# Performance work log

Measured on AMD Instinct MI355X. Metric: run time of the kernel, lower is better.

Reference implementation:

```python
import jax, jax.numpy as jnp
import numpy as np

ALPHA = 0.2      # leaky_relu negative slope
EPS = 1e-5       # BatchNorm eps
NEG = -9e15      # masked attention fill (matches -9000000000000000.0)


def _xavier(key, shape):
    fan_in, fan_out = shape[-2], shape[-1]
    lim = jnp.sqrt(6.0 / (fan_in + fan_out))
    return jax.random.uniform(key, shape, minval=-lim, maxval=lim, dtype=jnp.float32)


def setup_inputs() -> dict:
    key = jax.random.key(0)
    ks = jax.random.split(key, 10)
    b, N, L = 8, 1024, 4
    C, G, O, F = 128, 128, 64, 64   # n_feats, global_feats, global_out_feats, n_filters
    V = jax.random.normal(ks[0], (b, N, C), dtype=jnp.float32)
    A = jax.random.normal(ks[1], (b, N, L, N), dtype=jnp.float32)
    global_state = jax.random.normal(ks[2], (b, G), dtype=jnp.float32)
    graph_size = jax.random.randint(ks[3], (b,), 0, N, dtype=jnp.int32)
    subgraph_size = jax.random.randint(ks[4], (b, 1), 0, N, dtype=jnp.int32)
    Wg = _xavier(ks[5], (G, O))                 # broadcast_global_state.weights[0]
    W = _xavier(ks[6], (L, C + O, F))           # GAT per-channel weight_list
    a1 = _xavier(ks[7], (L, F, 1))
    a2 = _xavier(ks[8], (L, F, 1))
    bias_gat = jnp.full((F,), 0.01, dtype=jnp.float32)
    gamma_n = jnp.ones((F,), jnp.float32); beta_n = jnp.zeros((F,), jnp.float32)
    gamma_g = jnp.ones((O,), jnp.float32); beta_g = jnp.zeros((O,), jnp.float32)
    return dict(V=V, A=A, global_state=global_state, graph_size=graph_size,
                subgraph_size=subgraph_size, Wg=Wg, W=W, a1=a1, a2=a2,
                bias_gat=bias_gat, gamma_n=gamma_n, beta_n=beta_n,
                gamma_g=gamma_g, beta_g=beta_g)


def reference(V, A, global_state, graph_size, subgraph_size,
              Wg, W, a1, a2, bias_gat, gamma_n, beta_n, gamma_g, beta_g):
    b, N, C = V.shape
    # --- GraphNodeCatGlobalFeatures (mols=1): project global state, broadcast to
    # the first graph_size[i] nodes of each graph, zeros for padding nodes.
    gs = global_state @ Wg                                   # [b, O]
    node_mask = (jnp.arange(N)[None, :] < graph_size[:, None]).astype(V.dtype)  # [b, N]
    Vg = jnp.concatenate([V, gs[:, None, :] * node_mask[:, :, None]], axis=-1)  # [b, N, C+O]
    # --- GraphAttentionLayer, all adj channels vectorized. dropout=0.
    h = jnp.einsum('bnc,lcf->lbnf', Vg, W)                   # [L, b, N, F]
    f1 = jnp.einsum('lbnf,lf->lbn', h, a1[:, :, 0])          # [L, b, N]
    f2 = jnp.einsum('lbnf,lf->lbn', h, a2[:, :, 0])
    e = jax.nn.leaky_relu(f1[:, :, :, None] + f2[:, :, None, :], ALPHA)  # [L, b, N, N]
    adj = jnp.transpose(A, (2, 0, 1, 3))                     # [L, b, N, N]
    att = jnp.where(adj > 0, e, jnp.asarray(NEG, e.dtype))
    att = jax.nn.softmax(att, axis=2)                        # torch softmax dim=1 (row index)
    out = jnp.einsum('lbnm,lbmf->bnf', att, h) + bias_gat    # sum over channels, [b, N, F]
    # --- bn_graph (BatchNorm1d over feature channel, training-mode batch stats) + relu
    mu = out.mean(axis=(0, 1))
    var = out.var(axis=(0, 1))
    out = jax.nn.relu((out - mu) / jnp.sqrt(var + EPS) * gamma_n + beta_n)
    # --- bn_global + relu on the projected global state
    gmu = gs.mean(axis=0)
    gvar = gs.var(axis=0)
    gs_out = jax.nn.relu((gs - gmu) / jnp.sqrt(gvar + EPS) * gamma_g + beta_g)
    return (out, gs_out)
```

## Files before the change

kernel.cpp:

```cpp
#include <hip/hip_runtime.h>
#include <hip/hip_fp16.h>

typedef unsigned long long u64;
typedef unsigned short ushort_t;
typedef __attribute__((ext_vector_type(8))) short short8v;
typedef __attribute__((ext_vector_type(16))) float f32x16;

#define DI __device__ __forceinline__

DI unsigned cvt_pk_bf16(float lo, float hi) {
    unsigned r;
    asm volatile("v_cvt_pk_bf16_f32 %0, %1, %2" : "=v"(r) : "v"(lo), "v"(hi));
    return r;
}

__global__ __launch_bounds__(256)
void k_h(const float* V, const int* gsize, const float* gstate, const float* Wg,
         const float* W, const float* a1, const float* a2,
         ushort_t* hT, float* f1, float* f2)
{
    int blk = blockIdx.x;
    int b = blk >> 5, nt = blk & 31, n0 = nt * 32;
    int t = threadIdx.x;
    __shared__ float gss[64];
    __shared__ float was[2][4][192];
    __shared__ float vg[32][194];
    if (t < 64) {
        float acc = 0.f;
        for (int c = 0; c < 128; ++c) acc += gstate[b*128 + c] * Wg[c*64 + t];
        gss[t] = acc;
    } else {
        int tt = t - 64;
        #pragma unroll
        for (int k = 0; k < 8; ++k) {
            int e = tt + k*192;
            int which = (e >= 768) ? 1 : 0;
            int idx = which ? e - 768 : e;
            int l = idx / 192, c = idx - l*192;
            const float* ap = (which ? a2 : a1) + l*64;
            const float* wp = W + (l*192 + c) * 64;
            float s = 0.f;
            for (int f = 0; f < 64; ++f) s += wp[f] * ap[f];
            was[which][l][c] = s;
        }
    }
    __syncthreads();
    {
        int r = t >> 3, c0 = (t & 7) * 16;
        const float* vp = V + ((size_t)(b*1024 + n0 + r) * 128 + c0);
        float4 v0 = *(const float4*)(vp + 0);
        float4 v1 = *(const float4*)(vp + 4);
        float4 v2 = *(const float4*)(vp + 8);
        float4 v3 = *(const float4*)(vp + 12);
        *(float4*)&vg[r][c0 + 0]  = v0;
        *(float4*)&vg[r][c0 + 4]  = v1;
        *(float4*)&vg[r][c0 + 8]  = v2;
        *(float4*)&vg[r][c0 + 12] = v3;
    }
    {
        int r = t >> 3, o0 = (t & 7) * 8;
        bool on = (n0 + r) < gsize[b];
        for (int j = 0; j < 8; ++j) vg[r][128 + o0 + j] = on ? gss[o0 + j] : 0.f;
    }
    __syncthreads();
    int ty = t >> 5, tx = t & 31;
    int r0 = ty * 4;
    int j0 = tx * 8;
    int lw = j0 >> 6, f0 = j0 & 63;
    float acc[4][8];
    for (int i = 0; i < 4; ++i) for (int j = 0; j < 8; ++j) acc[i][j] = 0.f;
    const float* wp = W + (size_t)(lw*192) * 64 + f0;
    for (int c = 0; c < 192; ++c) {
        float4 wl = *(const float4*)(wp + c*64);
        float4 wh = *(const float4*)(wp + c*64 + 4);
        float wf[8] = {wl.x, wl.y, wl.z, wl.w, wh.x, wh.y, wh.z, wh.w};
        float a0 = vg[r0+0][c], a1v = vg[r0+1][c], a2v = vg[r0+2][c], a3v = vg[r0+3][c];
        for (int j = 0; j < 8; ++j) {
            acc[0][j] += a0  * wf[j];
            acc[1][j] += a1v * wf[j];
            acc[2][j] += a2v * wf[j];
            acc[3][j] += a3v * wf[j];
        }
    }
    int lb = lw*8 + b;
    #pragma unroll
    for (int j = 0; j < 8; ++j) {
        uint2 st;
        st.x = cvt_pk_bf16(acc[0][j], acc[1][j]);
        st.y = cvt_pk_bf16(acc[2][j], acc[3][j]);
        *(uint2*)(hT + ((size_t)(lb*64 + f0 + j)) * 1024 + n0 + r0) = st;
    }
    {
        int r = t & 31, l = (t >> 5) & 3, which = t >> 7;
        const float* wl = &was[which][l][0];
        float s = 0.f;
        for (int c = 0; c < 192; ++c) s += vg[r][c] * wl[c];
        float* dst = which ? f2 : f1;
        dst[(l*8 + b) * 1024 + n0 + r] = s;
    }
}

__global__ __launch_bounds__(256, 2)
void k_maskcolsum(const float* A, const float* f1, const float* f2,
                  u64* maskp, float* psum)
{
    int blk = blockIdx.x;
    int nc = blk & 15, l = (blk >> 4) & 3, b = blk >> 6;
    int t = threadIdx.x;
    int wv = t >> 6, lane = t & 63;
    int lb = l*8 + b;
    int n0 = nc*64 + wv*16;
    ushort_t* mp16 = (ushort_t*)maskp;

    float K[16], F2r[16];
    {
        const float* f2p = f2 + lb*1024 + lane*16;
        #pragma unroll
        for (int q = 0; q < 4; ++q) {
            float4 v = *(const float4*)(f2p + q*4);
            float x4[4] = {v.x, v.y, v.z, v.w};
            #pragma unroll
            for (int i = 0; i < 4; ++i) {
                F2r[q*4 + i] = x4[i];
                K[q*4 + i]   = fmaxf(x4[i], 0.2f*x4[i]) + 12.f;
            }
        }
    }
    float f1r[16];
    {
        const float* f1p = f1 + lb*1024 + n0;
        #pragma unroll
        for (int q = 0; q < 4; ++q) {
            float4 v = *(const float4*)(f1p + q*4);
            f1r[q*4+0] = v.x; f1r[q*4+1] = v.y; f1r[q*4+2] = v.z; f1r[q*4+3] = v.w;
        }
    }
    float s[16];
    #pragma unroll
    for (int j = 0; j < 16; ++j) s[j] = 0.f;

    const float* Abase = A + (((size_t)(b*1024 + n0) * 4 + l) * 1024) + lane*16;

    auto LOADB = [&](float4* dst, int batch) {
        #pragma unroll
        for (int r = 0; r < 4; ++r) {
            const float* ap = Abase + (size_t)(batch*4 + r) * 4096;
            dst[r*4+0] = *(const float4*)(ap + 0);
            dst[r*4+1] = *(const float4*)(ap + 4);
            dst[r*4+2] = *(const float4*)(ap + 8);
            dst[r*4+3] = *(const float4*)(ap + 12);
        }
    };
    auto PROC = [&](float4* src, int batch) {
        #pragma unroll
        for (int r = 0; r < 4; ++r) {
            int n = n0 + batch*4 + r;
            float f1n = f1r[batch*4 + r];
            unsigned bits = 0;
            #pragma unroll
            for (int q = 0; q < 4; ++q) {
                float4 v = src[r*4 + q];
                float x4[4] = {v.x, v.y, v.z, v.w};
                #pragma unroll
                for (int i = 0; i < 4; ++i) {
                    int j = q*4 + i;
                    bool pos = x4[i] > 0.f;
                    bits |= pos ? (1u << j) : 0u;
                    float x = f1n + F2r[j];
                    x = fmaxf(x, 0.2f * x);
                    float p = __expf(x - K[j]);
                    s[j] += pos ? p : 0.f;
                }
            }
            mp16[(((size_t)(b*1024 + n) * 4 + l) << 6) + lane] = (ushort_t)bits;
        }
    };

    float4 Abuf[16], Bbuf[16];
    LOADB(Abuf, 0);
    LOADB(Bbuf, 1);
    PROC(Abuf, 0);
    LOADB(Abuf, 2);
    PROC(Bbuf, 1);
    LOADB(Bbuf, 3);
    PROC(Abuf, 2);
    PROC(Bbuf, 3);

    __shared__ float ss[4][64][17];
    #pragma unroll
    for (int j = 0; j < 16; ++j) ss[wv][lane][j] = s[j];
    __syncthreads();
    #pragma unroll
    for (int q = 0; q < 4; ++q) {
        int m = q*256 + t;
        int l2 = m >> 4, j = m & 15;
        float v = (ss[0][l2][j] + ss[1][l2][j]) + (ss[2][l2][j] + ss[3][l2][j]);
        psum[(size_t)nc*32768 + lb*1024 + m] = v;
    }
}

__global__ __launch_bounds__(256)
void k_csum(const float* psum, const float* f2, float* ecol, float* base)
{
    int i = blockIdx.x * 256 + threadIdx.x;
    float s = 0.f;
    #pragma unroll
    for (int k = 0; k < 16; ++k) s += psum[(size_t)k*32768 + i];
    float x = f2[i];
    float K = fmaxf(x, 0.2f*x) + 12.f;
    bool emp = (s == 0.f);
    ecol[i] = emp ? 0.f : __expf(-K) / s;
    base[i] = emp ? (1.f/1024.f) : 0.f;
}

__global__ __launch_bounds__(256)
void k_pass2(const ushort_t* hT, const u64* maskp, const float* f1,
             const float* f2, const float* ecol, const float* base, __half* outl2)
{
    int blk = blockIdx.x;
    int nt = blk & 7, b = (blk >> 3) & 7, l = (blk >> 6) & 3, ks = blk >> 8;
    int lb = l*8 + b;
    int n0 = nt*128;
    int m0 = ks*512;
    int t = threadIdx.x;
    int w = t >> 6, lane = t & 63;
    int rl = lane & 31, kg = lane >> 5;

    __shared__ float f2t[512], ect[512], bat[512];
    __shared__ ushort_t hl[64][72];

    for (int k = 0; k < 2; ++k) {
        int j = t + k*256;
        f2t[j] = f2[lb*1024 + m0 + j];
        ect[j] = ecol[lb*1024 + m0 + j];
        bat[j] = base[lb*1024 + m0 + j];
    }
    int nrow = n0 + w*32 + rl;
    float f1v = f1[lb*1024 + nrow];
    const u64* mrow = maskp + ((size_t)(b*1024 + nrow)*4 + l)*16 + ks*8;

    f32x16 acc0 = {0,0,0,0,0,0,0,0,0,0,0,0,0,0,0,0};
    f32x16 acc1 = {0,0,0,0,0,0,0,0,0,0,0,0,0,0,0,0};

    int hf = t >> 2, hseg = t & 3;
    const ushort_t* hsrc = hT + ((size_t)(lb*64 + hf)) * 1024 + m0 + hseg*16;

    for (int kc = 0; kc < 8; ++kc) {
        __syncthreads();
        {
            const uint4* s = (const uint4*)(hsrc + kc*64);
            uint4 q0 = s[0], q1 = s[1];
            *(uint4*)&hl[hf][hseg*16]     = q0;
            *(uint4*)&hl[hf][hseg*16 + 8] = q1;
        }
        u64 wm = mrow[kc];
        __syncthreads();
        #pragma unroll
        for (int kk = 0; kk < 4; ++kk) {
            int jb = kc*64 + kk*16 + kg*8;
            float4 fa = *(float4*)&f2t[jb];
            float4 fb = *(float4*)&f2t[jb+4];
            float4 ea = *(float4*)&ect[jb];
            float4 eb = *(float4*)&ect[jb+4];
            float4 ba = *(float4*)&bat[jb];
            float4 bb = *(float4*)&bat[jb+4];
            unsigned mb = (unsigned)(wm >> (kk*16 + kg*8)) & 0xffu;
            float xs[8] = {fa.x,fa.y,fa.z,fa.w,fb.x,fb.y,fb.z,fb.w};
            float es[8] = {ea.x,ea.y,ea.z,ea.w,eb.x,eb.y,eb.z,eb.w};
            float bs[8] = {ba.x,ba.y,ba.z,ba.w,bb.x,bb.y,bb.z,bb.w};
            float av[8];
            #pragma unroll
            for (int i = 0; i < 8; ++i) {
                float x = f1v + xs[i];
                x = fmaxf(x, 0.2f * x);
                float p = __expf(x) * es[i];
                av[i] = (mb & (1u << i)) ? p : bs[i];
            }
            union { unsigned u[4]; short8v s; } af;
            af.u[0] = cvt_pk_bf16(av[0], av[1]);
            af.u[1] = cvt_pk_bf16(av[2], av[3]);
            af.u[2] = cvt_pk_bf16(av[4], av[5]);
            af.u[3] = cvt_pk_bf16(av[6], av[7]);
            short8v b0 = *(short8v*)&hl[rl][kk*16 + kg*8];
            short8v b1 = *(short8v*)&hl[32 + rl][kk*16 + kg*8];
            acc0 = __builtin_amdgcn_mfma_f32_32x32x16_bf16(af.s, b0, acc0, 0, 0, 0);
            acc1 = __builtin_amdgcn_mfma_f32_32x32x16_bf16(af.s, b1, acc1, 0, 0, 0);
        }
    }
    int sl = ks*4 + l;
    __half* op = outl2 + ((size_t)(sl*8 + b) * 1024) * 64;
    #pragma unroll
    for (int r = 0; r < 16; ++r) {
        int row = n0 + w*32 + (r & 3) + 8*(r >> 2) + 4*kg;
        op[(size_t)row*64 + rl]      = __float2half(acc0[r]);
        op[(size_t)row*64 + 32 + rl] = __float2half(acc1[r]);
    }
}

__global__ __launch_bounds__(256)
void k_reduce(const __half* outl2, const float* bias, float* outpre, float* bnsum, float* bnsumsq)
{
    int blk = blockIdx.x, t = threadIdx.x;
    __shared__ float red[2][64];
    if (t < 128) red[t >> 6][t & 63] = 0.f;
    __syncthreads();
    size_t idx = (size_t)blk * 2048 + t * 8;
    int fb = (t * 8) & 63;
    float o[8];
    for (int j = 0; j < 8; ++j) o[j] = bias[fb + j];
    #pragma unroll
    for (int sl = 0; sl < 8; ++sl) {
        uint4 u = *(const uint4*)(outl2 + (size_t)sl * 524288 + idx);
        const __half* hh = (const __half*)&u;
        #pragma unroll
        for (int j = 0; j < 8; ++j) o[j] += __half2float(hh[j]);
    }
    *(float4*)(outpre + idx)     = make_float4(o[0], o[1], o[2], o[3]);
    *(float4*)(outpre + idx + 4) = make_float4(o[4], o[5], o[6], o[7]);
    for (int j = 0; j < 8; ++j) {
        atomicAdd(&red[0][fb + j], o[j]);
        atomicAdd(&red[1][fb + j], o[j]*o[j]);
    }
    __syncthreads();
    if (t < 64) { atomicAdd(&bnsum[t], red[0][t]); atomicAdd(&bnsumsq[t], red[1][t]); }
}

__global__ __launch_bounds__(256)
void k_bnapply(const float* outpre, const float* bnsum, const float* bnsumsq,
               const float* gamma, const float* beta, float* out,
               const float* gstate, const float* Wg,
               const float* gamma_g, const float* beta_g, float* out_gs)
{
    int blk = blockIdx.x, t = threadIdx.x;
    __shared__ float gsa[512];
    __shared__ float gmu[64], grs[64];
    if (blk == 0) {
        for (int p = t; p < 512; p += 256) {
            int bb = p >> 6, o = p & 63;
            float acc = 0.f;
            for (int c = 0; c < 128; ++c) acc += gstate[bb*128 + c] * Wg[c*64 + o];
            gsa[p] = acc;
        }
        __syncthreads();
        if (t < 64) {
            float s = 0.f, sq = 0.f;
            for (int bb = 0; bb < 8; ++bb) { float v = gsa[bb*64 + t]; s += v; sq += v*v; }
            float mu = s * 0.125f;
            float var = sq * 0.125f - mu*mu;
            gmu[t] = mu; grs[t] = rsqrtf(var + 1e-5f);
        }
        __syncthreads();
        for (int p = t; p < 512; p += 256) {
            int o = p & 63;
            float v = (gsa[p] - gmu[o]) * grs[o] * gamma_g[o] + beta_g[o];
            out_gs[p] = fmaxf(v, 0.f);
        }
    }
    int f0 = (t * 4) & 63;
    float mu[4], rstd[4], ga[4], be[4];
    for (int j = 0; j < 4; ++j) {
        float sm = bnsum[f0 + j], sq = bnsumsq[f0 + j];
        float m = sm * (1.f / 8192.f);
        float var = sq * (1.f / 8192.f) - m*m;
        mu[j] = m; rstd[j] = rsqrtf(var + 1e-5f);
        ga[j] = gamma[f0 + j]; be[j] = beta[f0 + j];
    }
    for (int g = 0; g < 4; ++g) {
        size_t base = (size_t)blk * 4096 + g * 1024 + t * 4;
        float4 v = *(const float4*)(outpre + base);
        float x[4] = {v.x, v.y, v.z, v.w};
        float y[4];
        for (int j = 0; j < 4; ++j) {
            float z = (x[j] - mu[j]) * rstd[j] * ga[j] + be[j];
            y[j] = fmaxf(z, 0.f);
        }
        *(float4*)(out + base) = make_float4(y[0], y[1], y[2], y[3]);
    }
}

extern "C" void kernel_launch(void* const* d_in, const int* in_sizes, int n_in,
                              void* d_out, int out_size, void* d_ws, size_t ws_size,
                              hipStream_t stream)
{
    const float* V       = (const float*)d_in[0];
    const float* A       = (const float*)d_in[1];
    const float* gstate  = (const float*)d_in[2];
    const int*   gsize   = (const int*)d_in[3];
    const float* Wg      = (const float*)d_in[5];
    const float* W       = (const float*)d_in[6];
    const float* a1      = (const float*)d_in[7];
    const float* a2      = (const float*)d_in[8];
    const float* bias    = (const float*)d_in[9];
    const float* gamma_n = (const float*)d_in[10];
    const float* beta_n  = (const float*)d_in[11];
    const float* gamma_g = (const float*)d_in[12];
    const float* beta_g  = (const float*)d_in[13];

    char* ws = (char*)d_ws;
    float*    f1      = (float*)(ws + 0);
    float*    f2      = (float*)(ws + 131072);
    float*    ecol    = (float*)(ws + 262144);
    float*    base    = (float*)(ws + 393216);
    float*    bnsum   = (float*)(ws + 524288);
    float*    bnsumsq = (float*)(ws + 524544);
    u64*      maskp   = (u64*)  (ws + 525312);
    ushort_t* hT      = (ushort_t*)(ws + 4719616);
    float*    psum    = (float*)(ws + 8913920);
    __half*   outl2   = (__half*)(ws + 11011072);
    float*    outpre  = (float*)(ws + 19399680);

    float* out_main = (float*)d_out;
    float* out_gs   = out_main + 524288;

    (void)hipMemsetAsync(bnsum, 0, 512, stream);
    hipLaunchKernelGGL(k_h,          dim3(256),  dim3(256), 0, stream,
                       V, gsize, gstate, Wg, W, a1, a2, hT, f1, f2);
    hipLaunchKernelGGL(k_maskcolsum, dim3(512),  dim3(256), 0, stream,
                       A, f1, f2, maskp, psum);
    hipLaunchKernelGGL(k_csum,       dim3(128),  dim3(256), 0, stream,
                       psum, f2, ecol, base);
    hipLaunchKernelGGL(k_pass2,      dim3(512),  dim3(256), 0, stream,
                       hT, maskp, f1, f2, ecol, base, outl2);
    hipLaunchKernelGGL(k_reduce,     dim3(256),  dim3(256), 0, stream,
                       outl2, bias, outpre, bnsum, bnsumsq);
    hipLaunchKernelGGL(k_bnapply,    dim3(128),  dim3(256), 0, stream,
                       outpre, bnsum, bnsumsq, gamma_n, beta_n, out_main,
                       gstate, Wg, gamma_g, beta_g, out_gs);
}
```

Measured before the change: 136.8 us.

## Split fused mask/colsum kernel into streaming mask kernel and colsum kernel

Replaces the fused kernel, which read the 128 MB adjacency tensor while also computing the masked exp column sums, with two kernels. A simple high-occupancy streaming kernel packs the sign mask into 16-bit words. A second kernel reads the compact mask and computes the column sums. The intent is to let the large A read run at full bandwidth without register-heavy compute limiting occupancy, at the cost of an extra launch and a 4 MB mask round trip.

```diff
diff --git a/kernel.cpp b/kernel.cpp
--- a/kernel.cpp
+++ b/kernel.cpp
@@ -100,9 +100,37 @@
     }
 }
 
-__global__ __launch_bounds__(256, 2)
-void k_maskcolsum(const float* A, const float* f1, const float* f2,
-                  u64* maskp, float* psum)
+__global__ __launch_bounds__(256)
+void k_mask(const float* A, ushort_t* mask16)
+{
+    size_t i = (size_t)blockIdx.x * 256 + threadIdx.x;
+    const float4* p = (const float4*)(A + i * 16);
+    float4 a0 = p[0];
+    float4 a1 = p[1];
+    float4 a2 = p[2];
+    float4 a3 = p[3];
+    unsigned bits = 0;
+    bits |= (a0.x > 0.f) ? 1u << 0  : 0u;
+    bits |= (a0.y > 0.f) ? 1u << 1  : 0u;
+    bits |= (a0.z > 0.f) ? 1u << 2  : 0u;
+    bits |= (a0.w > 0.f) ? 1u << 3  : 0u;
+    bits |= (a1.x > 0.f) ? 1u << 4  : 0u;
+    bits |= (a1.y > 0.f) ? 1u << 5  : 0u;
+    bits |= (a1.z > 0.f) ? 1u << 6  : 0u;
+    bits |= (a1.w > 0.f) ? 1u << 7  : 0u;
+    bits |= (a2.x > 0.f) ? 1u << 8  : 0u;
+    bits |= (a2.y > 0.f) ? 1u << 9  : 0u;
+    bits |= (a2.z > 0.f) ? 1u << 10 : 0u;
+    bits |= (a2.w > 0.f) ? 1u << 11 : 0u;
+    bits |= (a3.x > 0.f) ? 1u << 12 : 0u;
+    bits |= (a3.y > 0.f) ? 1u << 13 : 0u;
+    bits |= (a3.z > 0.f) ? 1u << 14 : 0u;
+    bits |= (a3.w > 0.f) ? 1u << 15 : 0u;
+    mask16[i] = (ushort_t)bits;
+}
+
+__global__ __launch_bounds__(256)
+void k_colsum(const ushort_t* mask16, const float* f1, const float* f2, float* psum)
 {
     int blk = blockIdx.x;
     int nc = blk & 15, l = (blk >> 4) & 3, b = blk >> 6;
@@ -110,7 +138,6 @@
     int wv = t >> 6, lane = t & 63;
     int lb = l*8 + b;
     int n0 = nc*64 + wv*16;
-    ushort_t* mp16 = (ushort_t*)maskp;
 
     float K[16], F2r[16];
     {
@@ -135,57 +162,26 @@
             f1r[q*4+0] = v.x; f1r[q*4+1] = v.y; f1r[q*4+2] = v.z; f1r[q*4+3] = v.w;
         }
     }
+    const ushort_t* mp = mask16 + (((size_t)(b*1024 + n0) * 4 + l) << 6) + lane;
+    unsigned wbits[16];
+    #pragma unroll
+    for (int r = 0; r < 16; ++r) wbits[r] = mp[(size_t)r * 256];
+
     float s[16];
     #pragma unroll
     for (int j = 0; j < 16; ++j) s[j] = 0.f;
-
-    const float* Abase = A + (((size_t)(b*1024 + n0) * 4 + l) * 1024) + lane*16;
-
-    auto LOADB = [&](float4* dst, int batch) {
-        #pragma unroll
-        for (int r = 0; r < 4; ++r) {
-            const float* ap = Abase + (size_t)(batch*4 + r) * 4096;
-            dst[r*4+0] = *(const float4*)(ap + 0);
-            dst[r*4+1] = *(const float4*)(ap + 4);
-            dst[r*4+2] = *(const float4*)(ap + 8);
-            dst[r*4+3] = *(const float4*)(ap + 12);
-        }
-    };
-    auto PROC = [&](float4* src, int batch) {
-        #pragma unroll
-        for (int r = 0; r < 4; ++r) {
-            int n = n0 + batch*4 + r;
-            float f1n = f1r[batch*4 + r];
-            unsigned bits = 0;
-            #pragma unroll
-            for (int q = 0; q < 4; ++q) {
-                float4 v = src[r*4 + q];
-                float x4[4] = {v.x, v.y, v.z, v.w};
-                #pragma unroll
-                for (int i = 0; i < 4; ++i) {
-                    int j = q*4 + i;
-                    bool pos = x4[i] > 0.f;
-                    bits |= pos ? (1u << j) : 0u;
-                    float x = f1n + F2r[j];
-                    x = fmaxf(x, 0.2f * x);
-                    float p = __expf(x - K[j]);
-                    s[j] += pos ? p : 0.f;
-                }
-            }
-            mp16[(((size_t)(b*1024 + n) * 4 + l) << 6) + lane] = (ushort_t)bits;
-        }
-    };
-
-    float4 Abuf[16], Bbuf[16];
-    LOADB(Abuf, 0);
-    LOADB(Bbuf, 1);
-    PROC(Abuf, 0);
-    LOADB(Abuf, 2);
-    PROC(Bbuf, 1);
-    LOADB(Bbuf, 3);
-    PROC(Abuf, 2);
-    PROC(Bbuf, 3);
-
+    #pragma unroll
+    for (int r = 0; r < 16; ++r) {
+        unsigned bits = wbits[r];
+        float f1n = f1r[r];
+        #pragma unroll
+        for (int j = 0; j < 16; ++j) {
+            float x = f1n + F2r[j];
+            x = fmaxf(x, 0.2f * x);
+            float p = __expf(x - K[j]);
+            s[j] += ((bits >> j) & 1u) ? p : 0.f;
+        }
+    }
     __shared__ float ss[4][64][17];
     #pragma unroll
     for (int j = 0; j < 16; ++j) ss[wv][lane][j] = s[j];
@@ -413,17 +409,19 @@
     float* out_gs   = out_main + 524288;
 
     (void)hipMemsetAsync(bnsum, 0, 512, stream);
-    hipLaunchKernelGGL(k_h,          dim3(256),  dim3(256), 0, stream,
+    hipLaunchKernelGGL(k_h,       dim3(256),  dim3(256), 0, stream,
                        V, gsize, gstate, Wg, W, a1, a2, hT, f1, f2);
-    hipLaunchKernelGGL(k_maskcolsum, dim3(512),  dim3(256), 0, stream,
-                       A, f1, f2, maskp, psum);
-    hipLaunchKernelGGL(k_csum,       dim3(128),  dim3(256), 0, stream,
+    hipLaunchKernelGGL(k_mask,    dim3(8192), dim3(256), 0, stream,
+                       A, (ushort_t*)maskp);
+    hipLaunchKernelGGL(k_colsum,  dim3(512),  dim3(256), 0, stream,
+                       (const ushort_t*)maskp, f1, f2, psum);
+    hipLaunchKernelGGL(k_csum,    dim3(128),  dim3(256), 0, stream,
                        psum, f2, ecol, base);
-    hipLaunchKernelGGL(k_pass2,      dim3(512),  dim3(256), 0, stream,
+    hipLaunchKernelGGL(k_pass2,   dim3(512),  dim3(256), 0, stream,
                        hT, maskp, f1, f2, ecol, base, outl2);
-    hipLaunchKernelGGL(k_reduce,     dim3(256),  dim3(256), 0, stream,
+    hipLaunchKernelGGL(k_reduce,  dim3(256),  dim3(256), 0, stream,
                        outl2, bias, outpre, bnsum, bnsumsq);
-    hipLaunchKernelGGL(k_bnapply,    dim3(128),  dim3(256), 0, stream,
+    hipLaunchKernelGGL(k_bnapply, dim3(128),  dim3(256), 0, stream,
                        outpre, bnsum, bnsumsq, gamma_n, beta_n, out_main,
                        gstate, Wg, gamma_g, beta_g, out_gs);
 }
```

Measured after the change: 123.9 us (median of 2 runs). 1.1x faster.
